# Performance work log

Hardware: AMD Instinct MI355X
Metric: run time of the kernel (lower is better)

Reference implementation:

```python
import jax, jax.numpy as jnp
import numpy as np
from jax import lax

NPOINT = 1024
RADIUS = 0.2
NSAMPLE = 32
BN_EPS = 1e-5


def farthest_point_sample(xyz, npoint):
    # xyz: (B, N, 3). Deterministic start at index 0 (torch uses randint).
    B, N, _ = xyz.shape

    def step(carry, _):
        distance, farthest = carry
        centroid = jnp.take_along_axis(xyz, farthest[:, None, None], axis=1)  # (B,1,3)
        d = jnp.sum((xyz - centroid) ** 2, axis=-1)  # (B,N)
        distance = jnp.minimum(distance, d)
        return (distance, jnp.argmax(distance, axis=-1).astype(jnp.int32)), farthest

    init = (jnp.full((B, N), 1e10, xyz.dtype), jnp.zeros((B,), jnp.int32))
    _, idxs = lax.scan(step, init, None, length=npoint)  # (npoint, B)
    return jnp.transpose(idxs)  # (B, npoint)


def square_distance(src, dst):
    # src: (B,S,3), dst: (B,N,3) -> (B,S,N) squared distances
    d = -2.0 * jnp.einsum('bsc,bnc->bsn', src, dst)
    d = d + jnp.sum(src ** 2, axis=-1)[:, :, None]
    d = d + jnp.sum(dst ** 2, axis=-1)[:, None, :]
    return d


def query_ball_point(radius, nsample, xyz, new_xyz):
    B, N, _ = xyz.shape
    S = new_xyz.shape[1]
    sqrdists = square_distance(new_xyz, xyz)  # (B,S,N)
    idx = jnp.broadcast_to(jnp.arange(N, dtype=jnp.int32), (B, S, N))
    idx = jnp.where(sqrdists > radius ** 2, N, idx)
    idx = jnp.sort(idx, axis=-1)[:, :, :nsample]  # (B,S,K)
    first = idx[:, :, :1]
    return jnp.where(idx == N, first, idx)


# batched gather: points (B,N,C), idx (B,...) -> (B,...,C)
_gather = jax.vmap(lambda p, i: p[i])


def bn_relu(x, gamma, beta):
    # training-mode BatchNorm2d over (B, C, S, K): stats over axes (0,2,3)
    m = jnp.mean(x, axis=(0, 2, 3), keepdims=True)
    v = jnp.var(x, axis=(0, 2, 3), keepdims=True)
    y = (x - m) * lax.rsqrt(v + BN_EPS)
    return jax.nn.relu(y * gamma[None, :, None, None] + beta[None, :, None, None])


def reference(xyz, points, W0, b0, g0, be0, W1, b1, g1, be1, W2, b2, g2, be2):
    # xyz: (B,3,N), points: (B,C,N)
    xyz_t = jnp.transpose(xyz, (0, 2, 1))      # (B,N,3)
    pts_t = jnp.transpose(points, (0, 2, 1))   # (B,N,C)

    fps_idx = farthest_point_sample(xyz_t, NPOINT)          # (B,S)
    new_xyz = _gather(xyz_t, fps_idx)                        # (B,S,3)
    group_idx = query_ball_point(RADIUS, NSAMPLE, xyz_t, new_xyz)  # (B,S,K)

    grouped_xyz = _gather(xyz_t, group_idx) - new_xyz[:, :, None, :]  # (B,S,K,3)
    grouped_pts = _gather(pts_t, group_idx)                           # (B,S,K,C)
    feat = jnp.concatenate([grouped_xyz, grouped_pts], axis=-1)      # (B,S,K,C+3)

    x = jnp.transpose(feat, (0, 3, 1, 2))  # (B, C+3, S, K)
    for W, b, g, be in ((W0, b0, g0, be0), (W1, b1, g1, be1), (W2, b2, g2, be2)):
        x = bn_relu(jnp.einsum('bcsk,oc->bosk', x, W) + b[None, :, None, None], g, be)
    new_points = jnp.max(x, axis=-1)  # (B, C_out, S)

    return jnp.transpose(new_xyz, (0, 2, 1)), new_points


def setup_inputs() -> dict:
    key = jax.random.key(0)
    ks = jax.random.split(key, 8)
    B, C_in, N = 16, 6, 4096
    inp = {
        'xyz': jax.random.uniform(ks[0], (B, 3, N), dtype=jnp.float32),
        'points': jax.random.normal(ks[1], (B, C_in, N), dtype=jnp.float32),
        'W0': 0.1 * jax.random.normal(ks[2], (32, C_in + 3), dtype=jnp.float32),
        'b0': 0.1 * jax.random.normal(ks[3], (32,), dtype=jnp.float32),
        'g0': jnp.ones((32,), jnp.float32),
        'be0': jnp.zeros((32,), jnp.float32),
        'W1': 0.1 * jax.random.normal(ks[4], (32, 32), dtype=jnp.float32),
        'b1': 0.1 * jax.random.normal(ks[5], (32,), dtype=jnp.float32),
        'g1': jnp.ones((32,), jnp.float32),
        'be1': jnp.zeros((32,), jnp.float32),
        'W2': 0.1 * jax.random.normal(ks[6], (64, 32), dtype=jnp.float32),
        'b2': 0.1 * jax.random.normal(ks[7], (64,), dtype=jnp.float32),
        'g2': jnp.ones((64,), jnp.float32),
        'be2': jnp.zeros((64,), jnp.float32),
    }
    return inp
```

## Files before the change

### kernel.cpp

```cpp
#include <hip/hip_runtime.h>

#define BATCH   16
#define NPTS    4096
#define NPOINT  1024
#define NSAMPLE 32
#define NSITES  (BATCH*NPOINT*NSAMPLE)


__device__ __forceinline__ float wave_max_bcast(float x) {
    int v = __float_as_int(x);
    int t;
    t = __builtin_amdgcn_update_dpp(v, v, 0x111, 0xf, 0xf, false);
    v = __float_as_int(fmaxf(__int_as_float(v), __int_as_float(t)));
    t = __builtin_amdgcn_update_dpp(v, v, 0x112, 0xf, 0xf, false);
    v = __float_as_int(fmaxf(__int_as_float(v), __int_as_float(t)));
    t = __builtin_amdgcn_update_dpp(v, v, 0x114, 0xf, 0xf, false);
    v = __float_as_int(fmaxf(__int_as_float(v), __int_as_float(t)));
    t = __builtin_amdgcn_update_dpp(v, v, 0x118, 0xf, 0xf, false);
    v = __float_as_int(fmaxf(__int_as_float(v), __int_as_float(t)));
    t = __builtin_amdgcn_update_dpp(v, v, 0x142, 0xa, 0xf, false);
    v = __float_as_int(fmaxf(__int_as_float(v), __int_as_float(t)));
    t = __builtin_amdgcn_update_dpp(v, v, 0x143, 0xc, 0xf, false);
    v = __float_as_int(fmaxf(__int_as_float(v), __int_as_float(t)));
    return __int_as_float(__builtin_amdgcn_readlane(v, 63));
}

__global__ __launch_bounds__(512, 1) void fps_kernel(
    const float* __restrict__ xyz,
    float* __restrict__ nxyz,
    float* __restrict__ out0)
{
    __shared__ float sx[NPTS], sy[NPTS], sz[NPTS];
    __shared__ int   s_sel[NPOINT];
    __shared__ unsigned long long redK[8];
    __shared__ alignas(16) float bc[4];

    const int b = blockIdx.x;
    const int t = threadIdx.x;
    const int wave = t >> 6, lane = t & 63;
    const float* xb = xyz + (size_t)b * 3 * NPTS;

    for (int i = t; i < NPTS; i += 512) {
        sx[i] = xb[i]; sy[i] = xb[NPTS+i]; sz[i] = xb[2*NPTS+i];
    }
    if (t == 0) s_sel[0] = 0;
    __syncthreads();

    const int base = t * 8;
    float px[8], py[8], pz[8], dist[8];
    #pragma unroll
    for (int j = 0; j < 8; ++j) {
        px[j] = sx[base+j]; py[j] = sy[base+j]; pz[j] = sz[base+j];
        dist[j] = 1e10f;
    }

    float cx = sx[0], cy = sy[0], cz = sz[0];
    for (int it = 0; it < NPOINT; ++it) {
        #pragma unroll
        for (int j = 0; j < 8; ++j) {
            const float dx = __fsub_rn(px[j], cx);
            const float dy = __fsub_rn(py[j], cy);
            const float dz = __fsub_rn(pz[j], cz);
            const float d  = __fadd_rn(__fadd_rn(__fmul_rn(dx,dx), __fmul_rn(dy,dy)),
                                       __fmul_rn(dz,dz));
            dist[j] = fminf(dist[j], d);
        }
        float tv0, tv1, tv2, tv3; int ti0, ti1, ti2, ti3;
        { bool c = dist[1] > dist[0]; tv0 = c ? dist[1] : dist[0]; ti0 = c ? 1 : 0; }
        { bool c = dist[3] > dist[2]; tv1 = c ? dist[3] : dist[2]; ti1 = c ? 3 : 2; }
        { bool c = dist[5] > dist[4]; tv2 = c ? dist[5] : dist[4]; ti2 = c ? 5 : 4; }
        { bool c = dist[7] > dist[6]; tv3 = c ? dist[7] : dist[6]; ti3 = c ? 7 : 6; }
        float nv0, nv1; int ni0, ni1;
        { bool c = tv1 > tv0; nv0 = c ? tv1 : tv0; ni0 = c ? ti1 : ti0; }
        { bool c = tv3 > tv2; nv1 = c ? tv3 : tv2; ni1 = c ? ti3 : ti2; }
        float bm; int bj;
        { bool c = nv1 > nv0; bm = c ? nv1 : nv0; bj = c ? ni1 : ni0; }
        const float M = wave_max_bcast(bm);
        const unsigned long long mask = __ballot(bm == M);
        const int wl = __ffsll((long long)mask) - 1;
        if (lane == wl) {
            const unsigned idxg = (unsigned)(base + bj);
            redK[wave] = ((unsigned long long)__float_as_uint(bm) << 32)
                         | (unsigned)(~idxg);
        }
        __syncthreads();
        if (wave == 0) {
            const unsigned long long k0 = redK[0], k1 = redK[1];
            const unsigned long long k2 = redK[2], k3 = redK[3];
            const unsigned long long k4 = redK[4], k5 = redK[5];
            const unsigned long long k6 = redK[6], k7 = redK[7];
            const unsigned long long a0 = (k1 > k0) ? k1 : k0;
            const unsigned long long a1 = (k3 > k2) ? k3 : k2;
            const unsigned long long a2 = (k5 > k4) ? k5 : k4;
            const unsigned long long a3 = (k7 > k6) ? k7 : k6;
            const unsigned long long b0_ = (a1 > a0) ? a1 : a0;
            const unsigned long long b1_ = (a3 > a2) ? a3 : a2;
            const unsigned long long km  = (b1_ > b0_) ? b1_ : b0_;
            const int far = (int)((~(unsigned)km) & (NPTS-1));
            const float fx = sx[far], fy = sy[far], fz = sz[far];
            if (lane == 0) {
                if (it + 1 < NPOINT) s_sel[it + 1] = far;
                *(float4*)bc = make_float4(fx, fy, fz, 0.f);
            }
        }
        __syncthreads();
        const float4 B = *(const float4*)bc;
        cx = B.x; cy = B.y; cz = B.z;
    }
    __syncthreads();
    for (int s = t; s < NPOINT; s += 512) {
        const int id = s_sel[s];
        const float x = sx[id], y = sy[id], z = sz[id];
        nxyz[((size_t)b*NPOINT + s)*3 + 0] = x;
        nxyz[((size_t)b*NPOINT + s)*3 + 1] = y;
        nxyz[((size_t)b*NPOINT + s)*3 + 2] = z;
        out0[(size_t)b*3*NPOINT + 0*NPOINT + s] = x;
        out0[(size_t)b*3*NPOINT + 1*NPOINT + s] = y;
        out0[(size_t)b*3*NPOINT + 2*NPOINT + s] = z;
    }
}

__global__ __launch_bounds__(256) void ball_kernel(
    const float* __restrict__ xyz, const float* __restrict__ nxyz,
    int* __restrict__ gidx)
{
    __shared__ float sx[NPTS], sy[NPTS], sz[NPTS];
    const int b  = blockIdx.x >> 4;
    const int sg = blockIdx.x & 15;
    const int t = threadIdx.x;
    const int wave = t >> 6, lane = t & 63;
    const float* xb = xyz + (size_t)b * 3 * NPTS;
    for (int i = t; i < NPTS; i += 256) {
        sx[i] = xb[i]; sy[i] = xb[NPTS+i]; sz[i] = xb[2*NPTS+i];
    }
    __syncthreads();
    const unsigned long long lt = (1ull << lane) - 1ull;

    for (int q = wave; q < 64; q += 4) {
        const int s = sg*64 + q;
        const size_t bs = (size_t)b*NPOINT + s;
        const float cx = nxyz[bs*3+0], cy = nxyz[bs*3+1], cz = nxyz[bs*3+2];
        const float ss = __fadd_rn(__fadd_rn(__fmul_rn(cx,cx), __fmul_rn(cy,cy)),
                                   __fmul_rn(cz,cz));
        int* out = gidx + bs*NSAMPLE;
        int cnt = 0;
        int firstIdx = NPTS;
        for (int ch = 0; ch < NPTS/64 && cnt < NSAMPLE; ++ch) {
            const int pi = ch*64 + lane;
            const float qx = sx[pi], qy = sy[pi], qz = sz[pi];
            const float dot = fmaf(cz, qz, fmaf(cy, qy, __fmul_rn(cx, qx)));
            const float sn  = __fadd_rn(__fadd_rn(__fmul_rn(qx,qx), __fmul_rn(qy,qy)),
                                        __fmul_rn(qz,qz));
            const float d   = __fadd_rn(__fadd_rn(__fmul_rn(-2.0f,dot), ss), sn);
            const bool pred = !(d > 0.04f);
            const unsigned long long m = __ballot(pred);
            if (pred) {
                const int pos = cnt + __popcll(m & lt);
                if (pos == 0) firstIdx = pi;
                if (pos < NSAMPLE) out[pos] = pi;
            }
            cnt += (int)__popcll(m);
        }
        if (cnt < NSAMPLE) {
            #pragma unroll
            for (int off = 32; off >= 1; off >>= 1) {
                const int oi = __shfl_xor(firstIdx, off);
                firstIdx = (oi < firstIdx) ? oi : firstIdx;
            }
            for (int p = cnt + lane; p < NSAMPLE; p += 64) out[p] = firstIdx;
        }
    }
}

__device__ __forceinline__ void gather_feat(
    const float* __restrict__ xyz, const float* __restrict__ pts,
    const int* __restrict__ gidx, const float* __restrict__ nxyz,
    int v, float4 f[9])
{
    const int site = v * 4;
    const int bs = site >> 5;
    const int b  = bs >> 10;
    const int4 idx = *reinterpret_cast<const int4*>(gidx + site);
    const float* xb = xyz + (size_t)b*3*NPTS;
    const float* pb = pts + (size_t)b*6*NPTS;
    const float cx = nxyz[(size_t)bs*3+0];
    const float cy = nxyz[(size_t)bs*3+1];
    const float cz = nxyz[(size_t)bs*3+2];
    f[0] = make_float4(xb[idx.x]-cx, xb[idx.y]-cx, xb[idx.z]-cx, xb[idx.w]-cx);
    f[1] = make_float4(xb[NPTS+idx.x]-cy, xb[NPTS+idx.y]-cy, xb[NPTS+idx.z]-cy, xb[NPTS+idx.w]-cy);
    f[2] = make_float4(xb[2*NPTS+idx.x]-cz, xb[2*NPTS+idx.y]-cz, xb[2*NPTS+idx.z]-cz, xb[2*NPTS+idx.w]-cz);
    #pragma unroll
    for (int c = 0; c < 6; ++c)
        f[3+c] = make_float4(pb[c*NPTS+idx.x], pb[c*NPTS+idx.y], pb[c*NPTS+idx.z], pb[c*NPTS+idx.w]);
}

__global__ __launch_bounds__(256) void conv0s_kernel(
    const float* __restrict__ xyz, const float* __restrict__ pts,
    const int* __restrict__ gidx, const float* __restrict__ nxyz,
    const float* __restrict__ W, const float* __restrict__ bias,
    float* __restrict__ xout, float* __restrict__ psum, float* __restrict__ psq)
{
    const int t = threadIdx.x;
    const int v = blockIdx.x*256 + t;
    const int site = v * 4;
    float4 f[9];
    gather_feat(xyz, pts, gidx, nxyz, v, f);
    float acc[32], accq[32];
    #pragma unroll
    for (int o = 0; o < 32; ++o) {
        const float bb = bias[o];
        float4 y = make_float4(bb,bb,bb,bb);
        #pragma unroll
        for (int c = 0; c < 9; ++c) {
            const float w = W[o*9+c];
            y.x = fmaf(w, f[c].x, y.x); y.y = fmaf(w, f[c].y, y.y);
            y.z = fmaf(w, f[c].z, y.z); y.w = fmaf(w, f[c].w, y.w);
        }
        *reinterpret_cast<float4*>(xout + (size_t)o*NSITES + site) = y;
        acc[o]  = (y.x + y.y) + (y.z + y.w);
        accq[o] = (y.x*y.x + y.y*y.y) + (y.z*y.z + y.w*y.w);
    }
    __shared__ float ls[4][32], lq[4][32];
    const int wave = t>>6, lane = t&63;
    #pragma unroll
    for (int o = 0; o < 32; ++o) {
        float s1 = acc[o], q1 = accq[o];
        #pragma unroll
        for (int off = 32; off >= 1; off >>= 1) {
            s1 += __shfl_xor(s1, off);
            q1 += __shfl_xor(q1, off);
        }
        if (lane == 0) { ls[wave][o] = s1; lq[wave][o] = q1; }
    }
    __syncthreads();
    if (t < 32) {
        psum[blockIdx.x*64 + t] = (ls[0][t]+ls[1][t]) + (ls[2][t]+ls[3][t]);
        psq [blockIdx.x*64 + t] = (lq[0][t]+lq[1][t]) + (lq[2][t]+lq[3][t]);
    }
}

__global__ void fold_kernel(
    const float* __restrict__ g, const float* __restrict__ be,
    const float* __restrict__ psum, const float* __restrict__ psq,
    float* __restrict__ aff, int Cout)
{
    __shared__ float ss[4][64], qq[4][64];
    const int t = threadIdx.x;
    const int ch = t & 63, part = t >> 6;
    float s = 0.f, q = 0.f;
    for (int i = part; i < 512; i += 4) {
        s += psum[i*64 + ch];
        q += psq [i*64 + ch];
    }
    ss[part][ch] = s; qq[part][ch] = q;
    __syncthreads();
    if (t < Cout) {
        s = (ss[0][t]+ss[1][t]) + (ss[2][t]+ss[3][t]);
        q = (qq[0][t]+qq[1][t]) + (qq[2][t]+qq[3][t]);
        const float invn = 1.0f / (float)NSITES;
        const float m = s * invn;
        float v2 = fmaxf(q * invn - m*m, 0.f);
        const float a = g[t] * rsqrtf(v2 + 1e-5f);
        aff[t]      = a;
        aff[64 + t] = fmaf(-m, a, be[t]);
    }
}

__global__ __launch_bounds__(256) void conv1s_kernel(
    const float* x, float* xout,
    const float* __restrict__ aff, const float* __restrict__ W,
    const float* __restrict__ bias,
    float* __restrict__ psum, float* __restrict__ psq)
{
    const int t = threadIdx.x;
    const int v = blockIdx.x*256 + t;
    const int site = v * 4;
    float4 in[32];
    #pragma unroll
    for (int c = 0; c < 32; ++c) {
        float4 r = *reinterpret_cast<const float4*>(x + (size_t)c*NSITES + site);
        const float a = aff[c], cc = aff[64 + c];
        in[c].x = fmaxf(fmaf(a, r.x, cc), 0.f);
        in[c].y = fmaxf(fmaf(a, r.y, cc), 0.f);
        in[c].z = fmaxf(fmaf(a, r.z, cc), 0.f);
        in[c].w = fmaxf(fmaf(a, r.w, cc), 0.f);
    }
    float acc[32], accq[32];
    #pragma unroll
    for (int o = 0; o < 32; ++o) {
        const float bb = bias[o];
        float4 y = make_float4(bb,bb,bb,bb);
        #pragma unroll
        for (int c = 0; c < 32; ++c) {
            const float w = W[o*32+c];
            y.x = fmaf(w, in[c].x, y.x); y.y = fmaf(w, in[c].y, y.y);
            y.z = fmaf(w, in[c].z, y.z); y.w = fmaf(w, in[c].w, y.w);
        }
        *reinterpret_cast<float4*>(xout + (size_t)o*NSITES + site) = y;
        acc[o]  = (y.x + y.y) + (y.z + y.w);
        accq[o] = (y.x*y.x + y.y*y.y) + (y.z*y.z + y.w*y.w);
    }
    __shared__ float ls[4][32], lq[4][32];
    const int wave = t>>6, lane = t&63;
    #pragma unroll
    for (int o = 0; o < 32; ++o) {
        float s1 = acc[o], q1 = accq[o];
        #pragma unroll
        for (int off = 32; off >= 1; off >>= 1) {
            s1 += __shfl_xor(s1, off);
            q1 += __shfl_xor(q1, off);
        }
        if (lane == 0) { ls[wave][o] = s1; lq[wave][o] = q1; }
    }
    __syncthreads();
    if (t < 32) {
        psum[blockIdx.x*64 + t] = (ls[0][t]+ls[1][t]) + (ls[2][t]+ls[3][t]);
        psq [blockIdx.x*64 + t] = (lq[0][t]+lq[1][t]) + (lq[2][t]+lq[3][t]);
    }
}

__global__ __launch_bounds__(256) void conv2stats_kernel(
    const float* __restrict__ x, const float* __restrict__ aff,
    const float* __restrict__ W, const float* __restrict__ bias,
    float* __restrict__ psum, float* __restrict__ psq)
{
    const int t = threadIdx.x;
    const int v = blockIdx.x*256 + t;
    const int site = v * 4;
    const int coff = blockIdx.y * 32;
    float4 in[32];
    #pragma unroll
    for (int c = 0; c < 32; ++c) {
        float4 r = *reinterpret_cast<const float4*>(x + (size_t)c*NSITES + site);
        const float a = aff[c], cc = aff[64 + c];
        in[c].x = fmaxf(fmaf(a, r.x, cc), 0.f);
        in[c].y = fmaxf(fmaf(a, r.y, cc), 0.f);
        in[c].z = fmaxf(fmaf(a, r.z, cc), 0.f);
        in[c].w = fmaxf(fmaf(a, r.w, cc), 0.f);
    }
    float acc[32], accq[32];
    #pragma unroll
    for (int o = 0; o < 32; ++o) {
        const float bb = bias[coff + o];
        float4 y = make_float4(bb,bb,bb,bb);
        #pragma unroll
        for (int c = 0; c < 32; ++c) {
            const float w = W[(coff+o)*32 + c];
            y.x = fmaf(w, in[c].x, y.x); y.y = fmaf(w, in[c].y, y.y);
            y.z = fmaf(w, in[c].z, y.z); y.w = fmaf(w, in[c].w, y.w);
        }
        acc[o]  = (y.x + y.y) + (y.z + y.w);
        accq[o] = (y.x*y.x + y.y*y.y) + (y.z*y.z + y.w*y.w);
    }
    __shared__ float ls[4][32], lq[4][32];
    const int wave = t>>6, lane = t&63;
    #pragma unroll
    for (int o = 0; o < 32; ++o) {
        float s1 = acc[o], q1 = accq[o];
        #pragma unroll
        for (int off = 32; off >= 1; off >>= 1) {
            s1 += __shfl_xor(s1, off);
            q1 += __shfl_xor(q1, off);
        }
        if (lane == 0) { ls[wave][o] = s1; lq[wave][o] = q1; }
    }
    __syncthreads();
    if (t < 32) {
        psum[blockIdx.x*64 + coff + t] = (ls[0][t]+ls[1][t]) + (ls[2][t]+ls[3][t]);
        psq [blockIdx.x*64 + coff + t] = (lq[0][t]+lq[1][t]) + (lq[2][t]+lq[3][t]);
    }
}

__global__ __launch_bounds__(256) void conv2max_kernel(
    const float* __restrict__ x, const float* __restrict__ aff1,
    const float* __restrict__ aff2, const float* __restrict__ W,
    const float* __restrict__ bias, float* __restrict__ outp)
{
    const int gt = blockIdx.x*256 + threadIdx.x;
    const int wv = gt >> 6;
    const int lane = gt & 63;
    const int base = wv * 64;
    float in[32];
    #pragma unroll
    for (int c = 0; c < 32; ++c) {
        const float r = x[(size_t)c*NSITES + base + lane];
        in[c] = fmaxf(fmaf(aff1[c], r, aff1[64 + c]), 0.f);
    }
    const int bs = (base + lane) >> 5;
    const int b = bs >> 10, s = bs & 1023;
    float* dst = outp + (size_t)b*64*NPOINT + s;
    for (int o = 0; o < 64; ++o) {
        float z = bias[o];
        #pragma unroll
        for (int c = 0; c < 32; ++c)
            z = fmaf(W[o*32+c], in[c], z);
        float y = fmaxf(fmaf(aff2[o], z, aff2[64 + o]), 0.f);
        #pragma unroll
        for (int off = 16; off >= 1; off >>= 1)
            y = fmaxf(y, __shfl_xor(y, off));
        if ((lane & 31) == 0)
            dst[(size_t)o*NPOINT] = y;
    }
}

extern "C" void kernel_launch(void* const* d_in, const int* in_sizes, int n_in,
                              void* d_out, int out_size, void* d_ws, size_t ws_size,
                              hipStream_t stream) {
    (void)in_sizes; (void)n_in; (void)out_size; (void)ws_size;
    const float* xyz = (const float*)d_in[0];
    const float* pts = (const float*)d_in[1];
    const float* W0  = (const float*)d_in[2];
    const float* b0  = (const float*)d_in[3];
    const float* g0  = (const float*)d_in[4];
    const float* be0 = (const float*)d_in[5];
    const float* W1  = (const float*)d_in[6];
    const float* b1  = (const float*)d_in[7];
    const float* g1  = (const float*)d_in[8];
    const float* be1 = (const float*)d_in[9];
    const float* W2  = (const float*)d_in[10];
    const float* b2  = (const float*)d_in[11];
    const float* g2  = (const float*)d_in[12];
    const float* be2 = (const float*)d_in[13];
    float* out = (float*)d_out;
    char* ws = (char*)d_ws;
    float* nxyz = (float*)(ws + 0);
    int*   gidx = (int*)  (ws + 196608);
    float* psum = (float*)(ws + 2293760);
    float* psq  = (float*)(ws + 2424832);
    float* aff0 = (float*)(ws + 2555904);
    float* aff1 = (float*)(ws + 2556416);
    float* aff2 = (float*)(ws + 2556928);
    float* xbuf = (float*)(ws + 2557440);

    fps_kernel <<<16,  512, 0, stream>>>(xyz, nxyz, out);
    ball_kernel<<<256, 256, 0, stream>>>(xyz, nxyz, gidx);

    conv0s_kernel<<<512, 256, 0, stream>>>(xyz, pts, gidx, nxyz, W0, b0,
                                           xbuf, psum, psq);
    fold_kernel<<<1, 256, 0, stream>>>(g0, be0, psum, psq, aff0, 32);

    conv1s_kernel<<<512, 256, 0, stream>>>(xbuf, xbuf, aff0, W1, b1, psum, psq);
    fold_kernel<<<1, 256, 0, stream>>>(g1, be1, psum, psq, aff1, 32);

    conv2stats_kernel<<<dim3(512,2), 256, 0, stream>>>(xbuf, aff1, W2, b2,
                                                       psum, psq);
    fold_kernel<<<1, 256, 0, stream>>>(g2, be2, psum, psq, aff2, 64);

    conv2max_kernel<<<2048, 256, 0, stream>>>(xbuf, aff1, aff2, W2, b2,
                                              out + 49152);
}
```

Baseline: 1.081 ms.

## Halve FPS block size with redundant per-wave reduction; merge conv2 stats channel halves

The farthest-point-sampling kernel now runs 256 threads with 16 points each. Every wave reads the four per-wave candidates and reduces them itself, using a double-buffered shared array, so the second barrier and the broadcast through shared memory on each iteration are gone. The conv2 stats kernel now computes all 64 output channels per thread on 2 sites in 512-thread blocks, instead of splitting channels across two grid rows, so the input is read and normalized once rather than twice. The cost is more serial work per thread in the latency-bound FPS loop and higher register pressure in both kernels.

Result: slower. 1.389 ms (+28.5%).

```diff
diff --git a/kernel.cpp b/kernel.cpp
--- a/kernel.cpp
+++ b/kernel.cpp
@@ -25,39 +25,40 @@
     return __int_as_float(__builtin_amdgcn_readlane(v, 63));
 }
 
-__global__ __launch_bounds__(512, 1) void fps_kernel(
+__global__ __launch_bounds__(256, 1) void fps_kernel(
     const float* __restrict__ xyz,
     float* __restrict__ nxyz,
     float* __restrict__ out0)
 {
     __shared__ float sx[NPTS], sy[NPTS], sz[NPTS];
     __shared__ int   s_sel[NPOINT];
-    __shared__ unsigned long long redK[8];
-    __shared__ alignas(16) float bc[4];
+    __shared__ unsigned long long redK[2][4];
 
     const int b = blockIdx.x;
     const int t = threadIdx.x;
     const int wave = t >> 6, lane = t & 63;
     const float* xb = xyz + (size_t)b * 3 * NPTS;
 
-    for (int i = t; i < NPTS; i += 512) {
+    for (int i = t; i < NPTS; i += 256) {
         sx[i] = xb[i]; sy[i] = xb[NPTS+i]; sz[i] = xb[2*NPTS+i];
     }
-    if (t == 0) s_sel[0] = 0;
-    __syncthreads();
-
-    const int base = t * 8;
-    float px[8], py[8], pz[8], dist[8];
-    #pragma unroll
-    for (int j = 0; j < 8; ++j) {
+    __syncthreads();
+
+    const int base = t * 16;
+    float px[16], py[16], pz[16], dist[16];
+    #pragma unroll
+    for (int j = 0; j < 16; ++j) {
         px[j] = sx[base+j]; py[j] = sy[base+j]; pz[j] = sz[base+j];
+        asm volatile("" : "+v"(px[j]), "+v"(py[j]), "+v"(pz[j]));
         dist[j] = 1e10f;
     }
 
+    int far = 0;
     float cx = sx[0], cy = sy[0], cz = sz[0];
     for (int it = 0; it < NPOINT; ++it) {
-        #pragma unroll
-        for (int j = 0; j < 8; ++j) {
+        if (t == 0) s_sel[it] = far;
+        #pragma unroll
+        for (int j = 0; j < 16; ++j) {
             const float dx = __fsub_rn(px[j], cx);
             const float dy = __fsub_rn(py[j], cy);
             const float dz = __fsub_rn(pz[j], cz);
@@ -65,50 +66,49 @@
                                        __fmul_rn(dz,dz));
             dist[j] = fminf(dist[j], d);
         }
-        float tv0, tv1, tv2, tv3; int ti0, ti1, ti2, ti3;
-        { bool c = dist[1] > dist[0]; tv0 = c ? dist[1] : dist[0]; ti0 = c ? 1 : 0; }
-        { bool c = dist[3] > dist[2]; tv1 = c ? dist[3] : dist[2]; ti1 = c ? 3 : 2; }
-        { bool c = dist[5] > dist[4]; tv2 = c ? dist[5] : dist[4]; ti2 = c ? 5 : 4; }
-        { bool c = dist[7] > dist[6]; tv3 = c ? dist[7] : dist[6]; ti3 = c ? 7 : 6; }
-        float nv0, nv1; int ni0, ni1;
-        { bool c = tv1 > tv0; nv0 = c ? tv1 : tv0; ni0 = c ? ti1 : ti0; }
-        { bool c = tv3 > tv2; nv1 = c ? tv3 : tv2; ni1 = c ? ti3 : ti2; }
+        float w0[8]; int j0[8];
+        #pragma unroll
+        for (int k = 0; k < 8; ++k) {
+            const bool c = dist[2*k+1] > dist[2*k];
+            w0[k] = c ? dist[2*k+1] : dist[2*k];
+            j0[k] = c ? 2*k+1 : 2*k;
+        }
+        float w1[4]; int j1[4];
+        #pragma unroll
+        for (int k = 0; k < 4; ++k) {
+            const bool c = w0[2*k+1] > w0[2*k];
+            w1[k] = c ? w0[2*k+1] : w0[2*k];
+            j1[k] = c ? j0[2*k+1] : j0[2*k];
+        }
+        float w2[2]; int j2[2];
+        #pragma unroll
+        for (int k = 0; k < 2; ++k) {
+            const bool c = w1[2*k+1] > w1[2*k];
+            w2[k] = c ? w1[2*k+1] : w1[2*k];
+            j2[k] = c ? j1[2*k+1] : j1[2*k];
+        }
         float bm; int bj;
-        { bool c = nv1 > nv0; bm = c ? nv1 : nv0; bj = c ? ni1 : ni0; }
+        { const bool c = w2[1] > w2[0]; bm = c ? w2[1] : w2[0]; bj = c ? j2[1] : j2[0]; }
         const float M = wave_max_bcast(bm);
         const unsigned long long mask = __ballot(bm == M);
         const int wl = __ffsll((long long)mask) - 1;
+        const int par = it & 1;
         if (lane == wl) {
             const unsigned idxg = (unsigned)(base + bj);
-            redK[wave] = ((unsigned long long)__float_as_uint(bm) << 32)
-                         | (unsigned)(~idxg);
+            redK[par][wave] = ((unsigned long long)__float_as_uint(bm) << 32)
+                              | (unsigned)(~idxg);
         }
         __syncthreads();
-        if (wave == 0) {
-            const unsigned long long k0 = redK[0], k1 = redK[1];
-            const unsigned long long k2 = redK[2], k3 = redK[3];
-            const unsigned long long k4 = redK[4], k5 = redK[5];
-            const unsigned long long k6 = redK[6], k7 = redK[7];
-            const unsigned long long a0 = (k1 > k0) ? k1 : k0;
-            const unsigned long long a1 = (k3 > k2) ? k3 : k2;
-            const unsigned long long a2 = (k5 > k4) ? k5 : k4;
-            const unsigned long long a3 = (k7 > k6) ? k7 : k6;
-            const unsigned long long b0_ = (a1 > a0) ? a1 : a0;
-            const unsigned long long b1_ = (a3 > a2) ? a3 : a2;
-            const unsigned long long km  = (b1_ > b0_) ? b1_ : b0_;
-            const int far = (int)((~(unsigned)km) & (NPTS-1));
-            const float fx = sx[far], fy = sy[far], fz = sz[far];
-            if (lane == 0) {
-                if (it + 1 < NPOINT) s_sel[it + 1] = far;
-                *(float4*)bc = make_float4(fx, fy, fz, 0.f);
-            }
-        }
-        __syncthreads();
-        const float4 B = *(const float4*)bc;
-        cx = B.x; cy = B.y; cz = B.z;
-    }
-    __syncthreads();
-    for (int s = t; s < NPOINT; s += 512) {
+        const unsigned long long k0 = redK[par][0], k1 = redK[par][1];
+        const unsigned long long k2 = redK[par][2], k3 = redK[par][3];
+        const unsigned long long a0 = (k1 > k0) ? k1 : k0;
+        const unsigned long long a1 = (k3 > k2) ? k3 : k2;
+        const unsigned long long km = (a1 > a0) ? a1 : a0;
+        far = (int)((~(unsigned)km) & (NPTS-1));
+        cx = sx[far]; cy = sy[far]; cz = sz[far];
+    }
+    __syncthreads();
+    for (int s = t; s < NPOINT; s += 256) {
         const int id = s_sel[s];
         const float x = sx[id], y = sy[id], z = sz[id];
         nxyz[((size_t)b*NPOINT + s)*3 + 0] = x;
@@ -319,43 +319,40 @@
     }
 }
 
-__global__ __launch_bounds__(256) void conv2stats_kernel(
+__global__ __launch_bounds__(512, 1) void conv2stats_kernel(
     const float* __restrict__ x, const float* __restrict__ aff,
     const float* __restrict__ W, const float* __restrict__ bias,
     float* __restrict__ psum, float* __restrict__ psq)
 {
     const int t = threadIdx.x;
-    const int v = blockIdx.x*256 + t;
-    const int site = v * 4;
-    const int coff = blockIdx.y * 32;
-    float4 in[32];
+    const int v = blockIdx.x*512 + t;
+    const int site = v * 2;
+    float2 in[32];
     #pragma unroll
     for (int c = 0; c < 32; ++c) {
-        float4 r = *reinterpret_cast<const float4*>(x + (size_t)c*NSITES + site);
+        const float2 r = *reinterpret_cast<const float2*>(x + (size_t)c*NSITES + site);
         const float a = aff[c], cc = aff[64 + c];
         in[c].x = fmaxf(fmaf(a, r.x, cc), 0.f);
         in[c].y = fmaxf(fmaf(a, r.y, cc), 0.f);
-        in[c].z = fmaxf(fmaf(a, r.z, cc), 0.f);
-        in[c].w = fmaxf(fmaf(a, r.w, cc), 0.f);
-    }
-    float acc[32], accq[32];
-    #pragma unroll
-    for (int o = 0; o < 32; ++o) {
-        const float bb = bias[coff + o];
-        float4 y = make_float4(bb,bb,bb,bb);
+    }
+    float acc[64], accq[64];
+    #pragma unroll
+    for (int o = 0; o < 64; ++o) {
+        const float bb = bias[o];
+        float yx = bb, yy = bb;
         #pragma unroll
         for (int c = 0; c < 32; ++c) {
-            const float w = W[(coff+o)*32 + c];
-            y.x = fmaf(w, in[c].x, y.x); y.y = fmaf(w, in[c].y, y.y);
-            y.z = fmaf(w, in[c].z, y.z); y.w = fmaf(w, in[c].w, y.w);
-        }
-        acc[o]  = (y.x + y.y) + (y.z + y.w);
-        accq[o] = (y.x*y.x + y.y*y.y) + (y.z*y.z + y.w*y.w);
-    }
-    __shared__ float ls[4][32], lq[4][32];
+            const float w = W[o*32+c];
+            yx = fmaf(w, in[c].x, yx);
+            yy = fmaf(w, in[c].y, yy);
+        }
+        acc[o]  = yx + yy;
+        accq[o] = yx*yx + yy*yy;
+    }
+    __shared__ float ls[8][64], lq[8][64];
     const int wave = t>>6, lane = t&63;
     #pragma unroll
-    for (int o = 0; o < 32; ++o) {
+    for (int o = 0; o < 64; ++o) {
         float s1 = acc[o], q1 = accq[o];
         #pragma unroll
         for (int off = 32; off >= 1; off >>= 1) {
@@ -365,9 +362,11 @@
         if (lane == 0) { ls[wave][o] = s1; lq[wave][o] = q1; }
     }
     __syncthreads();
-    if (t < 32) {
-        psum[blockIdx.x*64 + coff + t] = (ls[0][t]+ls[1][t]) + (ls[2][t]+ls[3][t]);
-        psq [blockIdx.x*64 + coff + t] = (lq[0][t]+lq[1][t]) + (lq[2][t]+lq[3][t]);
+    if (t < 64) {
+        psum[blockIdx.x*64 + t] = ((ls[0][t]+ls[1][t]) + (ls[2][t]+ls[3][t]))
+                                + ((ls[4][t]+ls[5][t]) + (ls[6][t]+ls[7][t]));
+        psq [blockIdx.x*64 + t] = ((lq[0][t]+lq[1][t]) + (lq[2][t]+lq[3][t]))
+                                + ((lq[4][t]+lq[5][t]) + (lq[6][t]+lq[7][t]));
     }
 }
 
@@ -432,7 +431,7 @@
     float* aff2 = (float*)(ws + 2556928);
     float* xbuf = (float*)(ws + 2557440);
 
-    fps_kernel <<<16,  512, 0, stream>>>(xyz, nxyz, out);
+    fps_kernel <<<16,  256, 0, stream>>>(xyz, nxyz, out);
     ball_kernel<<<256, 256, 0, stream>>>(xyz, nxyz, gidx);
 
     conv0s_kernel<<<512, 256, 0, stream>>>(xyz, pts, gidx, nxyz, W0, b0,
@@ -442,8 +441,7 @@
     conv1s_kernel<<<512, 256, 0, stream>>>(xbuf, xbuf, aff0, W1, b1, psum, psq);
     fold_kernel<<<1, 256, 0, stream>>>(g1, be1, psum, psq, aff1, 32);
 
-    conv2stats_kernel<<<dim3(512,2), 256, 0, stream>>>(xbuf, aff1, W2, b2,
-                                                       psum, psq);
+    conv2stats_kernel<<<512, 512, 0, stream>>>(xbuf, aff1, W2, b2, psum, psq);
     fold_kernel<<<1, 256, 0, stream>>>(g2, be2, psum, psq, aff2, 64);
 
     conv2max_kernel<<<2048, 256, 0, stream>>>(xbuf, aff1, aff2, W2, b2,
```
